# Kernel tuning notes

Measured on AMD Instinct MI355X. Metric: run time of the kernel, lower is better.

## Reference

```python
import jax, jax.numpy as jnp
import numpy as np
from jax import lax

INPUT_DIM = 16
H1, H2 = 64, 32
OUT_DIM = 1
B, T = 4096, 168


def _uniform(key, shape, k):
    return jax.random.uniform(key, shape, jnp.float32, -k, k)


def setup_inputs() -> dict:
    key = jax.random.key(0)
    ks = jax.random.split(key, 12)
    k1 = 1.0 / np.sqrt(H1)
    k2 = 1.0 / np.sqrt(H2)
    return {
        "x": jax.random.normal(ks[0], (B, T, INPUT_DIM), jnp.float32),
        # layer 1 (PyTorch gate order: i, f, g, o)
        "W_ih1": _uniform(ks[1], (4 * H1, INPUT_DIM), k1),
        "W_hh1": _uniform(ks[2], (4 * H1, H1), k1),
        "b_ih1": _uniform(ks[3], (4 * H1,), k1),
        "b_hh1": _uniform(ks[4], (4 * H1,), k1),
        # layer 2
        "W_ih2": _uniform(ks[5], (4 * H2, H1), k2),
        "W_hh2": _uniform(ks[6], (4 * H2, H2), k2),
        "b_ih2": _uniform(ks[7], (4 * H2,), k2),
        "b_hh2": _uniform(ks[8], (4 * H2,), k2),
        # final linear
        "W_fc": _uniform(ks[9], (OUT_DIM, H2), k2),
        "b_fc": _uniform(ks[10], (OUT_DIM,), k2),
    }


def _lstm(x, W_ih, W_hh, b_ih, b_hh, hidden):
    # Precompute input-to-gate projections for all timesteps: [B, T, 4H]
    xg = jnp.einsum("btd,gd->btg", x, W_ih) + b_ih + b_hh

    def step(carry, xt):
        h, c = carry
        gates = xt + h @ W_hh.T  # [B, 4H]
        i, f, g, o = jnp.split(gates, 4, axis=-1)
        i = jax.nn.sigmoid(i)
        f = jax.nn.sigmoid(f)
        g = jnp.tanh(g)
        o = jax.nn.sigmoid(o)
        c = f * c + i * g
        h = o * jnp.tanh(c)
        return (h, c), h

    bsz = x.shape[0]
    init = (jnp.zeros((bsz, hidden), x.dtype), jnp.zeros((bsz, hidden), x.dtype))
    (_, _), hs = lax.scan(step, init, jnp.swapaxes(xg, 0, 1))  # hs: [T, B, H]
    return jnp.swapaxes(hs, 0, 1)  # [B, T, H]


def reference(x, W_ih1, W_hh1, b_ih1, b_hh1, W_ih2, W_hh2, b_ih2, b_hh2, W_fc, b_fc):
    # Dropout layers are identity at inference (p=0.2 in train only).
    h1 = _lstm(x, W_ih1, W_hh1, b_ih1, b_hh1, H1)   # [B, T, 64]
    h2 = _lstm(h1, W_ih2, W_hh2, b_ih2, b_hh2, H2)  # [B, T, 32]
    last = h2[:, -1, :]                              # [B, 32]
    return last @ W_fc.T + b_fc                      # [B, OUT_DIM]
```

## Files before the change

kernel.cpp:

```cpp
#include <hip/hip_runtime.h>


typedef __bf16 bf16x8 __attribute__((ext_vector_type(8)));
typedef float  f32x4  __attribute__((ext_vector_type(4)));

constexpr int T_SEQ = 168;
constexpr int NB    = 16;

__device__ __forceinline__ void split_fast(float x, __bf16& hi, __bf16& lo) {
  const unsigned u  = __float_as_uint(x);
  const unsigned hb = u & 0xFFFF0000u;
  const float    lf = x - __uint_as_float(hb);
  hi = __builtin_bit_cast(__bf16, (unsigned short)(hb >> 16));
  lo = __builtin_bit_cast(__bf16, (unsigned short)(__float_as_uint(lf) >> 16));
}

__device__ __forceinline__ void load_frag8(const float* __restrict__ Wrow, int k0,
                                           bf16x8& hi, bf16x8& lo) {
#pragma unroll
  for (int j = 0; j < 8; ++j) {
    float v = Wrow[k0 + j];
    __bf16 h = (__bf16)v;
    hi[j] = h;
    lo[j] = (__bf16)(v - (float)h);
  }
}

#define MFMA(a, b, c) __builtin_amdgcn_mfma_f32_16x16x32_bf16((a), (b), (c), 0, 0, 0)

__global__ __launch_bounds__(512) __attribute__((amdgpu_waves_per_eu(2, 2)))
void lstm_mfma_kernel(const float* __restrict__ x,
    const float* __restrict__ Wih1, const float* __restrict__ Whh1,
    const float* __restrict__ bih1, const float* __restrict__ bhh1,
    const float* __restrict__ Wih2, const float* __restrict__ Whh2,
    const float* __restrict__ bih2, const float* __restrict__ bhh2,
    const float* __restrict__ Wfc,  const float* __restrict__ bfc,
    float* __restrict__ out)
{
  __shared__ __align__(16) __bf16 sA1[2][4 * 64 * 8];
  __shared__ __align__(16) __bf16 sA2[2][2 * 64 * 8];
  __shared__ __align__(16) __bf16 sW2lo[8 * 2 * 64 * 8];
  __shared__ __align__(16) float  sP[2][2 * 4 * 64 * 4];
  __shared__ __align__(16) float  sXg[2][16 * 64 * 4];
  __shared__ __align__(16) float  sB2[8 * 64 * 4];
  __shared__ __align__(16) float  sH2f[16 * 32];

  const int tid  = threadIdx.x;
  const int w    = tid >> 6;
  const int lane = tid & 63;
  const int q    = lane >> 4;
  const int col  = lane & 15;
  const int b0   = blockIdx.x * NB;

  const bool isL1  = (w < 4);
  const bool isL2b = (w == 4) || (w == 5);
  const bool isL2a = (w >= 6);
  const int  wl2b  = w - 4;
  const int  wl2a  = w - 6;

  if (isL1) __builtin_amdgcn_s_setprio(1);

  const f32x4 z4 = {0.f, 0.f, 0.f, 0.f};

  bf16x8 bhh[4][4];
  f32x4  b1sd[4];
  if (isL1) {
#pragma unroll
    for (int g = 0; g < 4; ++g) {
      const int r = g * 64 + w * 16 + col;
      const float* Wr = Whh1 + r * 64;
      bf16x8 h0, l0, h1f, l1f;
      load_frag8(Wr, 0 * 32 + q * 8, h0, l0);
      load_frag8(Wr, 1 * 32 + q * 8, h1f, l1f);
      bhh[g][0] = h0; bhh[g][1] = h1f; bhh[g][2] = l0; bhh[g][3] = l1f;
      const float bv = bih1[r] + bhh1[r];
      b1sd[g][0] = bv; b1sd[g][1] = bv; b1sd[g][2] = bv; b1sd[g][3] = bv;
    }
  }
  bf16x8 wh2h[4], wh2l[4];
  if (isL2b) {
#pragma unroll
    for (int g = 0; g < 4; ++g) {
      const int r = g * 32 + wl2b * 16 + col;
      bf16x8 hh, ll;
      load_frag8(Whh2 + r * 32, q * 8, hh, ll);
      wh2h[g] = hh; wh2l[g] = ll;
      const float bv = bih2[r] + bhh2[r];
      f32x4 bs; bs[0] = bv; bs[1] = bv; bs[2] = bv; bs[3] = bv;
      *(f32x4*)&sB2[((wl2b * 4 + g) * 64 + lane) * 4] = bs;
    }
  }
  bf16x8 w2ih[4][2];
  bf16x8 xw[8];
  if (isL2a) {
#pragma unroll
    for (int g = 0; g < 4; ++g) {
      const int r = g * 32 + wl2a * 16 + col;
#pragma unroll
      for (int kb = 0; kb < 2; ++kb) {
        bf16x8 hh, ll;
        load_frag8(Wih2 + r * 64, kb * 32 + q * 8, hh, ll);
        w2ih[g][kb] = hh;
      }
    }
#pragma unroll
    for (int pp = 0; pp < 2; ++pp) {
#pragma unroll
      for (int g = 0; g < 4; ++g) {
        const int lw = wl2a * 2 + pp;
        const int r  = g * 64 + lw * 16 + col;
        bf16x8 hh, ll;
        load_frag8(Wih1 + r * 16, (q & 1) * 8, hh, ll);
        xw[pp * 4 + g] = (q < 2) ? hh : ll;
      }
    }
  }

  for (int idx = tid; idx < 8 * 2 * 64; idx += 512) {
    const int nt  = idx >> 7;
    const int kb2 = (idx >> 6) & 1;
    const int ln  = idx & 63;
    const int qq  = ln >> 4, cc = ln & 15;
    const int g   = nt >> 1, wv = nt & 1;
    const int r   = g * 32 + wv * 16 + cc;
    const int k0  = kb2 * 32 + qq * 8;
    bf16x8 hh, ll;
    load_frag8(Wih2 + r * 64, k0, hh, ll);
    *(bf16x8*)&sW2lo[((nt * 2 + kb2) * 64 + ln) * 8] = ll;
  }

  {
    bf16x8 z;
#pragma unroll
    for (int j = 0; j < 8; ++j) z[j] = (__bf16)0.f;
    for (int i = tid; i < 2 * 4 * 64; i += 512) *(bf16x8*)&sA1[0][i * 8] = z;
    for (int i = tid; i < 2 * 2 * 64; i += 512) *(bf16x8*)&sA2[0][i * 8] = z;
  }

  const float* xbase = x + ((size_t)(b0 + col) * T_SEQ) * 16 + (q & 1) * 8;
  float4 xcA, xcB;

#define XG_BODY(PDST, DO_PRE, TT) do {                                         \
      const float xcv[8] = {xcA.x, xcA.y, xcA.z, xcA.w, xcB.x, xcB.y, xcB.z, xcB.w}; \
      bf16x8 xh8, xl8;                                                         \
      _Pragma("unroll")                                                        \
      for (int j = 0; j < 8; ++j) {                                            \
        __bf16 h_, l_; split_fast(xcv[j], h_, l_);                             \
        xh8[j] = h_; xl8[j] = l_;                                              \
      }                                                                        \
      const bf16x8 ax0 = (q < 2) ? xh8 : xl8;                                  \
      const bf16x8 ax1 = (q < 2) ? xl8 : xh8;                                  \
      if (DO_PRE) {                                                            \
        const float* xr = xbase + (size_t)((TT) + 2) * 16;                     \
        xcA = *(const float4*)(xr + 0);                                        \
        xcB = *(const float4*)(xr + 4);                                        \
      }                                                                        \
      _Pragma("unroll")                                                        \
      for (int p = 0; p < 8; ++p) {                                            \
        f32x4 pa = MFMA(ax0, xw[p], z4);                                       \
        pa = MFMA(ax1, xw[p], pa);                                             \
        *(f32x4*)&sXg[(PDST)][(((wl2a * 2 + (p >> 2)) * 4 + (p & 3)) * 64 + lane) * 4] = pa; \
      }                                                                        \
  } while (0)

  if (isL2a) {
    xcA = *(const float4*)(xbase + 0);
    xcB = *(const float4*)(xbase + 4);
    XG_BODY(0, false, 0);
    xcA = *(const float4*)(xbase + 16);
    xcB = *(const float4*)(xbase + 20);
  }
  __syncthreads();

  float c1s[4] = {0.f, 0.f, 0.f, 0.f};
  float c2s[4] = {0.f, 0.f, 0.f, 0.f};
  const int uu   = w * 16 + col;
  const int uu2b = wl2b * 16 + col;

  const int kbh  = uu >> 5;
  const int lnb  = ((uu & 31) >> 3) * 16;
  const int jj   = uu & 7;
  const int lnb2 = ((uu2b & 31) >> 3) * 16;
  const int jj2  = uu2b & 7;

#define CELL_UPDATE(ai_, af_, ag_, ao_, cprev_, ccout_, hfout_) do {           \
    const float Ei_ = __expf(-(ai_));                                          \
    const float Ef_ = __expf(-(af_));                                          \
    const float Eg_ = __expf((ag_) + (ag_));                                   \
    const float Eo_ = __expf(-(ao_));                                          \
    const float t1_ = (1.f + Ei_) * (Eg_ + 1.f);                               \
    const float t2_ = 1.f + Ef_;                                               \
    const float num_ = fmaf((cprev_), t1_, (Eg_ - 1.f) * t2_);                 \
    const float cc_  = num_ * __builtin_amdgcn_rcpf(t1_ * t2_);                \
    (ccout_) = cc_;                                                            \
    const float Ec_ = __expf(fminf(cc_ + cc_, 60.f));                          \
    (hfout_) = (Ec_ - 1.f) * __builtin_amdgcn_rcpf((1.f + Eo_) * (Ec_ + 1.f)); \
  } while (0)

#define STEP(Pc, DO_L1, DO_XG, DO_XPRE, DO_L2A, DO_L2B, DO_H2F, TT) do {       \
    if ((DO_L1) && isL1) {                                                     \
      f32x4 sd[4];                                                             \
      _Pragma("unroll")                                                        \
      for (int g = 0; g < 4; ++g)                                              \
        sd[g] = *(const f32x4*)&sXg[(Pc)][((w * 4 + g) * 64 + lane) * 4];      \
      bf16x8 a1[4];                                                            \
      _Pragma("unroll")                                                        \
      for (int kb = 0; kb < 4; ++kb)                                           \
        a1[kb] = *(const bf16x8*)&sA1[(Pc)][(kb * 64 + lane) * 8];             \
      f32x4 ca[4], cb[4];                                                      \
      _Pragma("unroll")                                                        \
      for (int g = 0; g < 4; ++g) {                                            \
        ca[g] = MFMA(a1[0], bhh[g][0], sd[g]);                                 \
        ca[g] = MFMA(a1[1], bhh[g][1], ca[g]);                                 \
        cb[g] = MFMA(a1[2], bhh[g][0], b1sd[g]);                               \
        cb[g] = MFMA(a1[3], bhh[g][1], cb[g]);                                 \
        cb[g] = MFMA(a1[0], bhh[g][2], cb[g]);                                 \
        cb[g] = MFMA(a1[1], bhh[g][3], cb[g]);                                 \
      }                                                                        \
      _Pragma("unroll")                                                        \
      for (int r = 0; r < 4; ++r) {                                            \
        const float ai = ca[0][r] + cb[0][r];                                  \
        const float af = ca[1][r] + cb[1][r];                                  \
        const float ag = ca[2][r] + cb[2][r];                                  \
        const float ao = ca[3][r] + cb[3][r];                                  \
        float cc, hf;                                                          \
        CELL_UPDATE(ai, af, ag, ao, c1s[r], cc, hf);                           \
        c1s[r] = cc;                                                           \
        __bf16 hh_, hl_;                                                       \
        split_fast(hf, hh_, hl_);                                              \
        const int m = q * 4 + r;                                               \
        sA1[1 - (Pc)][((kbh * 64) + lnb + m) * 8 + jj]       = hh_;            \
        sA1[1 - (Pc)][(((2 + kbh) * 64) + lnb + m) * 8 + jj] = hl_;            \
      }                                                                        \
    }                                                                          \
    if (isL2a) {                                                               \
      if (DO_XG) XG_BODY(1 - (Pc), (DO_XPRE), TT);                             \
      if (DO_L2A) {                                                            \
        bf16x8 a2[4];                                                          \
        _Pragma("unroll")                                                      \
        for (int kb = 0; kb < 4; ++kb)                                         \
          a2[kb] = *(const bf16x8*)&sA1[(Pc)][(kb * 64 + lane) * 8];           \
        _Pragma("unroll")                                                      \
        for (int g = 0; g < 4; ++g) {                                          \
          const int nt = g * 2 + wl2a;                                         \
          const bf16x8 bb2 = *(const bf16x8*)&sW2lo[((nt * 2 + 0) * 64 + lane) * 8]; \
          const bf16x8 bb3 = *(const bf16x8*)&sW2lo[((nt * 2 + 1) * 64 + lane) * 8]; \
          const f32x4 bs = *(const f32x4*)&sB2[((wl2a * 4 + g) * 64 + lane) * 4]; \
          f32x4 pa;                                                            \
          pa = MFMA(a2[0], w2ih[g][0], bs);          \
          pa = MFMA(a2[1], w2ih[g][1], pa);                                    \
          pa = MFMA(a2[0], bb2, pa);                              \
          pa = MFMA(a2[1], bb3, pa);                                           \
          pa = MFMA(a2[2], w2ih[g][0], pa);                       \
          pa = MFMA(a2[3], w2ih[g][1], pa);                                    \
          *(f32x4*)&sP[(Pc)][((wl2a * 4 + g) * 64 + lane) * 4] = pa;           \
        }                                                                      \
      }                                                                        \
    }                                                                          \
    if ((DO_L2B) && isL2b) {                                                   \
      const bf16x8 ah0 = *(const bf16x8*)&sA2[1 - (Pc)][(0 * 64 + lane) * 8];  \
      const bf16x8 ah1 = *(const bf16x8*)&sA2[1 - (Pc)][(1 * 64 + lane) * 8];  \
      f32x4 c2[4];                                                             \
      _Pragma("unroll")                                                        \
      for (int g = 0; g < 4; ++g) {                                            \
        const f32x4 ps = *(const f32x4*)&sP[1 - (Pc)][((wl2b * 4 + g) * 64 + lane) * 4]; \
        c2[g] = MFMA(ah0, wh2h[g], ps);         \
        c2[g] = MFMA(ah1, wh2h[g], c2[g]);                                     \
        c2[g] = MFMA(ah0, wh2l[g], c2[g]);                                     \
      }                                                                        \
      _Pragma("unroll")                                                        \
      for (int r = 0; r < 4; ++r) {                                            \
        float cc, hf;                                                          \
        CELL_UPDATE(c2[0][r], c2[1][r], c2[2][r], c2[3][r], c2s[r], cc, hf);   \
        c2s[r] = cc;                                                           \
        __bf16 hh_, hl_;                                                       \
        split_fast(hf, hh_, hl_);                                              \
        const int m = q * 4 + r;                                               \
        sA2[(Pc)][((0 * 64) + lnb2 + m) * 8 + jj2] = hh_;                      \
        sA2[(Pc)][((1 * 64) + lnb2 + m) * 8 + jj2] = hl_;                      \
        if (DO_H2F) sH2f[m * 32 + uu2b] = hf;                                  \
      }                                                                        \
    }                                                                          \
    __syncthreads();                                                           \
  } while (0)

  STEP(0, true,  true,  true,  false, false, false, 0);
  STEP(1, true,  true,  true,  true,  false, false, 1);
  for (int t = 2; t < 166; t += 2) {
    STEP(0, true, true, true, true, true, false, t);
    STEP(1, true, true, true, true, true, false, t + 1);
  }
  STEP(0, true,  true,  false, true,  true,  false, 166);
  STEP(1, true,  false, false, true,  true,  false, 167);
  STEP(0, false, false, false, true,  true,  false, 168);
  STEP(1, false, false, false, false, true,  true,  169);
#undef STEP
#undef CELL_UPDATE
#undef XG_BODY

  if (tid < NB) {
    float s = bfc[0];
#pragma unroll
    for (int j = 0; j < 32; ++j) s = fmaf(Wfc[j], sH2f[tid * 32 + j], s);
    out[b0 + tid] = s;
  }
}

extern "C" void kernel_launch(void* const* d_in, const int* in_sizes, int n_in,
                              void* d_out, int out_size, void* d_ws, size_t ws_size,
                              hipStream_t stream) {
  (void)in_sizes; (void)n_in; (void)out_size; (void)d_ws; (void)ws_size;
  const float* x    = (const float*)d_in[0];
  const float* Wih1 = (const float*)d_in[1];
  const float* Whh1 = (const float*)d_in[2];
  const float* bih1 = (const float*)d_in[3];
  const float* bhh1 = (const float*)d_in[4];
  const float* Wih2 = (const float*)d_in[5];
  const float* Whh2 = (const float*)d_in[6];
  const float* bih2 = (const float*)d_in[7];
  const float* bhh2 = (const float*)d_in[8];
  const float* Wfc  = (const float*)d_in[9];
  const float* bfc  = (const float*)d_in[10];
  float* out = (float*)d_out;

  hipLaunchKernelGGL(lstm_mfma_kernel, dim3(4096 / NB), dim3(512), 0, stream,
                     x, Wih1, Whh1, bih1, bhh1, Wih2, Whh2, bih2, bhh2, Wfc, bfc, out);
}
```

Measured before the change: 268.7 us.

## Move x-gate projection to L2b waves and keep W_ih2 low halves in registers

The x-to-gate projection for layer 1 moves from the layer-2 input-projection waves (6,7) to the layer-2 recurrent waves (4,5), which rebalances per-step work across the wavefronts. The low-precision halves of W_ih2 now sit in registers of the L2a waves instead of being read from shared memory every step, so the sW2lo LDS buffer is removed. The cost is more register pressure on the L2a waves and a longer critical path on L2b waves, which now do both the projection and the recurrent cell update.

```diff
diff --git a/kernel.cpp b/kernel.cpp
--- a/kernel.cpp
+++ b/kernel.cpp
@@ -39,7 +39,6 @@
 {
   __shared__ __align__(16) __bf16 sA1[2][4 * 64 * 8];
   __shared__ __align__(16) __bf16 sA2[2][2 * 64 * 8];
-  __shared__ __align__(16) __bf16 sW2lo[8 * 2 * 64 * 8];
   __shared__ __align__(16) float  sP[2][2 * 4 * 64 * 4];
   __shared__ __align__(16) float  sXg[2][16 * 64 * 4];
   __shared__ __align__(16) float  sB2[8 * 64 * 4];
@@ -78,6 +77,7 @@
     }
   }
   bf16x8 wh2h[4], wh2l[4];
+  bf16x8 xw[8];
   if (isL2b) {
 #pragma unroll
     for (int g = 0; g < 4; ++g) {
@@ -89,25 +89,11 @@
       f32x4 bs; bs[0] = bv; bs[1] = bv; bs[2] = bv; bs[3] = bv;
       *(f32x4*)&sB2[((wl2b * 4 + g) * 64 + lane) * 4] = bs;
     }
-  }
-  bf16x8 w2ih[4][2];
-  bf16x8 xw[8];
-  if (isL2a) {
-#pragma unroll
-    for (int g = 0; g < 4; ++g) {
-      const int r = g * 32 + wl2a * 16 + col;
-#pragma unroll
-      for (int kb = 0; kb < 2; ++kb) {
-        bf16x8 hh, ll;
-        load_frag8(Wih2 + r * 64, kb * 32 + q * 8, hh, ll);
-        w2ih[g][kb] = hh;
-      }
-    }
 #pragma unroll
     for (int pp = 0; pp < 2; ++pp) {
 #pragma unroll
       for (int g = 0; g < 4; ++g) {
-        const int lw = wl2a * 2 + pp;
+        const int lw = wl2b * 2 + pp;
         const int r  = g * 64 + lw * 16 + col;
         bf16x8 hh, ll;
         load_frag8(Wih1 + r * 16, (q & 1) * 8, hh, ll);
@@ -115,18 +101,19 @@
       }
     }
   }
-
-  for (int idx = tid; idx < 8 * 2 * 64; idx += 512) {
-    const int nt  = idx >> 7;
-    const int kb2 = (idx >> 6) & 1;
-    const int ln  = idx & 63;
-    const int qq  = ln >> 4, cc = ln & 15;
-    const int g   = nt >> 1, wv = nt & 1;
-    const int r   = g * 32 + wv * 16 + cc;
-    const int k0  = kb2 * 32 + qq * 8;
-    bf16x8 hh, ll;
-    load_frag8(Wih2 + r * 64, k0, hh, ll);
-    *(bf16x8*)&sW2lo[((nt * 2 + kb2) * 64 + ln) * 8] = ll;
+  bf16x8 w2ih[4][2], w2lo[4][2];
+  if (isL2a) {
+#pragma unroll
+    for (int g = 0; g < 4; ++g) {
+      const int r = g * 32 + wl2a * 16 + col;
+#pragma unroll
+      for (int kb = 0; kb < 2; ++kb) {
+        bf16x8 hh, ll;
+        load_frag8(Wih2 + r * 64, kb * 32 + q * 8, hh, ll);
+        w2ih[g][kb] = hh;
+        w2lo[g][kb] = ll;
+      }
+    }
   }
 
   {
@@ -159,11 +146,11 @@
       for (int p = 0; p < 8; ++p) {                                            \
         f32x4 pa = MFMA(ax0, xw[p], z4);                                       \
         pa = MFMA(ax1, xw[p], pa);                                             \
-        *(f32x4*)&sXg[(PDST)][(((wl2a * 2 + (p >> 2)) * 4 + (p & 3)) * 64 + lane) * 4] = pa; \
+        *(f32x4*)&sXg[(PDST)][(((wl2b * 2 + (p >> 2)) * 4 + (p & 3)) * 64 + lane) * 4] = pa; \
       }                                                                        \
   } while (0)
 
-  if (isL2a) {
+  if (isL2b) {
     xcA = *(const float4*)(xbase + 0);
     xcB = *(const float4*)(xbase + 4);
     XG_BODY(0, false, 0);
@@ -233,52 +220,49 @@
         sA1[1 - (Pc)][(((2 + kbh) * 64) + lnb + m) * 8 + jj] = hl_;            \
       }                                                                        \
     }                                                                          \
-    if (isL2a) {                                                               \
+    if ((DO_L2A) && isL2a) {                                                   \
+      bf16x8 a2[4];                                                            \
+      _Pragma("unroll")                                                        \
+      for (int kb = 0; kb < 4; ++kb)                                           \
+        a2[kb] = *(const bf16x8*)&sA1[(Pc)][(kb * 64 + lane) * 8];             \
+      _Pragma("unroll")                                                        \
+      for (int g = 0; g < 4; ++g) {                                            \
+        const f32x4 bs = *(const f32x4*)&sB2[((wl2a * 4 + g) * 64 + lane) * 4]; \
+        f32x4 pa;                                                              \
+        pa = MFMA(a2[0], w2ih[g][0], bs);            \
+        pa = MFMA(a2[1], w2ih[g][1], pa);                                      \
+        pa = MFMA(a2[0], w2lo[g][0], pa);       \
+        pa = MFMA(a2[1], w2lo[g][1], pa);                                      \
+        pa = MFMA(a2[2], w2ih[g][0], pa);                         \
+        pa = MFMA(a2[3], w2ih[g][1], pa);                                      \
+        *(f32x4*)&sP[(Pc)][((wl2a * 4 + g) * 64 + lane) * 4] = pa;             \
+      }                                                                        \
+    }                                                                          \
+    if (isL2b) {                                                               \
       if (DO_XG) XG_BODY(1 - (Pc), (DO_XPRE), TT);                             \
-      if (DO_L2A) {                                                            \
-        bf16x8 a2[4];                                                          \
-        _Pragma("unroll")                                                      \
-        for (int kb = 0; kb < 4; ++kb)                                         \
-          a2[kb] = *(const bf16x8*)&sA1[(Pc)][(kb * 64 + lane) * 8];           \
+      if (DO_L2B) {                                                            \
+        const bf16x8 ah0 = *(const bf16x8*)&sA2[1 - (Pc)][(0 * 64 + lane) * 8]; \
+        const bf16x8 ah1 = *(const bf16x8*)&sA2[1 - (Pc)][(1 * 64 + lane) * 8]; \
+        f32x4 c2[4];                                                           \
         _Pragma("unroll")                                                      \
         for (int g = 0; g < 4; ++g) {                                          \
-          const int nt = g * 2 + wl2a;                                         \
-          const bf16x8 bb2 = *(const bf16x8*)&sW2lo[((nt * 2 + 0) * 64 + lane) * 8]; \
-          const bf16x8 bb3 = *(const bf16x8*)&sW2lo[((nt * 2 + 1) * 64 + lane) * 8]; \
-          const f32x4 bs = *(const f32x4*)&sB2[((wl2a * 4 + g) * 64 + lane) * 4]; \
-          f32x4 pa;                                                            \
-          pa = MFMA(a2[0], w2ih[g][0], bs);          \
-          pa = MFMA(a2[1], w2ih[g][1], pa);                                    \
-          pa = MFMA(a2[0], bb2, pa);                              \
-          pa = MFMA(a2[1], bb3, pa);                                           \
-          pa = MFMA(a2[2], w2ih[g][0], pa);                       \
-          pa = MFMA(a2[3], w2ih[g][1], pa);                                    \
-          *(f32x4*)&sP[(Pc)][((wl2a * 4 + g) * 64 + lane) * 4] = pa;           \
+          const f32x4 ps = *(const f32x4*)&sP[1 - (Pc)][((wl2b * 4 + g) * 64 + lane) * 4]; \
+          c2[g] = MFMA(ah0, wh2h[g], ps);       \
+          c2[g] = MFMA(ah1, wh2h[g], c2[g]);                                   \
+          c2[g] = MFMA(ah0, wh2l[g], c2[g]);                                   \
         }                                                                      \
-      }                                                                        \
-    }                                                                          \
-    if ((DO_L2B) && isL2b) {                                                   \
-      const bf16x8 ah0 = *(const bf16x8*)&sA2[1 - (Pc)][(0 * 64 + lane) * 8];  \
-      const bf16x8 ah1 = *(const bf16x8*)&sA2[1 - (Pc)][(1 * 64 + lane) * 8];  \
-      f32x4 c2[4];                                                             \
-      _Pragma("unroll")                                                        \
-      for (int g = 0; g < 4; ++g) {                                            \
-        const f32x4 ps = *(const f32x4*)&sP[1 - (Pc)][((wl2b * 4 + g) * 64 + lane) * 4]; \
-        c2[g] = MFMA(ah0, wh2h[g], ps);         \
-        c2[g] = MFMA(ah1, wh2h[g], c2[g]);                                     \
-        c2[g] = MFMA(ah0, wh2l[g], c2[g]);                                     \
-      }                                                                        \
-      _Pragma("unroll")                                                        \
-      for (int r = 0; r < 4; ++r) {                                            \
-        float cc, hf;                                                          \
-        CELL_UPDATE(c2[0][r], c2[1][r], c2[2][r], c2[3][r], c2s[r], cc, hf);   \
-        c2s[r] = cc;                                                           \
-        __bf16 hh_, hl_;                                                       \
-        split_fast(hf, hh_, hl_);                                              \
-        const int m = q * 4 + r;                                               \
-        sA2[(Pc)][((0 * 64) + lnb2 + m) * 8 + jj2] = hh_;                      \
-        sA2[(Pc)][((1 * 64) + lnb2 + m) * 8 + jj2] = hl_;                      \
-        if (DO_H2F) sH2f[m * 32 + uu2b] = hf;                                  \
+        _Pragma("unroll")                                                      \
+        for (int r = 0; r < 4; ++r) {                                          \
+          float cc, hf;                                                        \
+          CELL_UPDATE(c2[0][r], c2[1][r], c2[2][r], c2[3][r], c2s[r], cc, hf); \
+          c2s[r] = cc;                                                         \
+          __bf16 hh_, hl_;                                                     \
+          split_fast(hf, hh_, hl_);                                            \
+          const int m = q * 4 + r;                                             \
+          sA2[(Pc)][((0 * 64) + lnb2 + m) * 8 + jj2] = hh_;                    \
+          sA2[(Pc)][((1 * 64) + lnb2 + m) * 8 + jj2] = hl_;                    \
+          if (DO_H2F) sH2f[m * 32 + uu2b] = hf;                                \
+        }                                                                      \
       }                                                                        \
     }                                                                          \
     __syncthreads();                                                           \
```

Result: slower. 409.1 us (+52.2%).
